# Kernel optimization log

Measured on AMD Instinct MI355X. Metric: run time of the kernel, lower is better.

## Reference

```python
import jax, jax.numpy as jnp
import numpy as np

N_USER = 100000
N_ITEM = 50000
N = N_USER + N_ITEM
E = 2400000
D = 64
L = 3
B = 4096
NEG_SLOPE = 0.01  # nn.LeakyReLU() default


def setup_inputs() -> dict:
    key = jax.random.key(0)
    ks = jax.random.split(key, 12)
    return {
        "features": jax.random.normal(ks[0], (N, D), dtype=jnp.float32),
        "rows": jax.random.randint(ks[1], (E,), 0, N),
        "cols": jax.random.randint(ks[2], (E,), 0, N),
        "vals": jax.random.uniform(ks[3], (E,), dtype=jnp.float32) * 0.02,
        "users": jax.random.randint(ks[4], (B,), 0, N_USER),
        "items": jax.random.randint(ks[5], (B,), 0, N_ITEM),
        "W1": jax.random.normal(ks[6], (L, D, D), dtype=jnp.float32) * 0.1,
        "b1": jax.random.normal(ks[7], (L, D), dtype=jnp.float32) * 0.01,
        "W2": jax.random.normal(ks[8], (L, D, D), dtype=jnp.float32) * 0.1,
        "b2": jax.random.normal(ks[9], (L, D), dtype=jnp.float32) * 0.01,
        "Wt": jax.random.normal(ks[10], (D, (L + 1) * D), dtype=jnp.float32) * 0.05,
        "bt": jax.random.normal(ks[11], (D,), dtype=jnp.float32) * 0.01,
    }


def _spmm(rows, cols, vals, x):
    # COO SpMM: out[r] += vals[e] * x[cols[e]]
    msgs = vals[:, None] * x[cols]  # [E, D] gather + scale
    return jax.ops.segment_sum(msgs, rows, num_segments=N)


def reference(features, rows, cols, vals, users, items, W1, b1, W2, b2, Wt, bt):
    feats = features
    embs = [feats]
    for l in range(L):
        agg = _spmm(rows, cols, vals, feats)          # sparse.mm(graph, features)
        part1 = (agg + feats) @ W1[l].T + b1[l]       # (graph+selfLoop) @ f -> Linear
        part2 = (agg * feats) @ W2[l].T + b2[l]       # elementwise mul -> Linear
        feats = jax.nn.leaky_relu(part1 + part2, negative_slope=NEG_SLOPE)
        embs.append(feats)
    final_emb = jnp.concatenate(embs, axis=1)         # [N, (L+1)*D]
    user_emb = final_emb[users] @ Wt.T + bt           # [B, D]
    item_emb = final_emb[N_USER + items] @ Wt.T + bt  # [B, D]
    return jnp.sum(user_emb * item_emb, axis=1)       # [B]
```

## Files before the change

### kernel.cpp

```cpp
#include <hip/hip_runtime.h>

#define N_USER 100000
#define N_NODE 150000
#define N_EDGE 2400000
#define DIM 64
#define BPAIR 4096
#define NEG_SLOPE 0.01f
#define RPG 4
#define NGROUP (N_NODE / RPG)
#define EPAD_CAP (N_EDGE + 8 * N_NODE)


__global__ void count_rank_kernel(const int* __restrict__ rows, int* __restrict__ cnt,
                                  int* __restrict__ rank) {
    int i = blockIdx.x * blockDim.x + threadIdx.x;
    if (i < N_EDGE) rank[i] = atomicAdd(&cnt[rows[i]], 1);
}

__global__ void scan1_kernel(const int* __restrict__ cnt, int* __restrict__ incl,
                             int* __restrict__ bsums) {
    __shared__ int s[256];
    int t = threadIdx.x;
    int i = blockIdx.x * 256 + t;
    s[t] = (i < N_NODE) ? ((cnt[i] + 7) & ~7) : 0;
    __syncthreads();
    for (int off = 1; off < 256; off <<= 1) {
        int add = (t >= off) ? s[t - off] : 0;
        __syncthreads();
        s[t] += add;
        __syncthreads();
    }
    if (i < N_NODE) incl[i] = s[t];
    if (t == 255) bsums[blockIdx.x] = s[255];
}

__global__ void scan2_kernel(int* __restrict__ bsums, int nblk) {
    __shared__ int s[1024];
    int t = threadIdx.x;
    s[t] = (t < nblk) ? bsums[t] : 0;
    __syncthreads();
    for (int off = 1; off < 1024; off <<= 1) {
        int add = (t >= off) ? s[t - off] : 0;
        __syncthreads();
        s[t] += add;
        __syncthreads();
    }
    if (t < nblk) bsums[t] = s[t];
}

__global__ void scan3_kernel(int* __restrict__ row_ptr, const int* __restrict__ bsums) {
    int i = blockIdx.x * 256 + threadIdx.x;
    if (i == 0) row_ptr[0] = 0;
    if (i < N_NODE && blockIdx.x > 0) row_ptr[1 + i] += bsums[blockIdx.x - 1];
}

__global__ void scatter_kernel(const int* __restrict__ rows, const int* __restrict__ cols,
                               const float* __restrict__ vals, const int* __restrict__ rank,
                               const int* __restrict__ row_ptr, int2* __restrict__ edges) {
    int i = blockIdx.x * blockDim.x + threadIdx.x;
    if (i < N_EDGE) {
        int p = row_ptr[rows[i]] + rank[i];
        edges[p] = make_int2(cols[i], __float_as_int(vals[i]));
    }
}

__global__ __launch_bounds__(256) void layer_kernel(
    const int* __restrict__ row_ptr, const int2* __restrict__ edges,
    const float* __restrict__ fin, float* __restrict__ fout,
    const float* __restrict__ W1l, const float* __restrict__ b1l,
    const float* __restrict__ W2l, const float* __restrict__ b2l) {
    __shared__ float h1s[4][RPG][64];
    __shared__ float h2s[4][RPG][64];
    int t = threadIdx.x;
    int wave = t >> 6, lane = t & 63;
    int gw = (blockIdx.x * 256 + t) >> 6;
    int nw = (gridDim.x * 256) >> 6;
    float bsum = b1l[lane] + b2l[lane];
    const float4* __restrict__ w1r = (const float4*)(W1l + (size_t)lane * 64);
    const float4* __restrict__ w2r = (const float4*)(W2l + (size_t)lane * 64);
    for (int g = gw; g < NGROUP; g += nw) {
        int r0 = g * RPG;
        int4 rp = *(const int4*)(row_ptr + r0);
        int rlast = row_ptr[r0 + 4];
        int eb[5] = {rp.x, rp.y, rp.z, rp.w, rlast};
#pragma unroll
        for (int m = 0; m < RPG; ++m) {
            int r = r0 + m;
            float f = fin[((size_t)r << 6) | lane];
            float a0 = 0.f, a1 = 0.f;
            for (int j = eb[m]; j < eb[m + 1]; j += 8) {
                int4 p0 = *(const int4*)(edges + j);
                int4 p1 = *(const int4*)(edges + j + 2);
                int4 p2 = *(const int4*)(edges + j + 4);
                int4 p3 = *(const int4*)(edges + j + 6);
                float g0 = fin[((size_t)p0.x << 6) | lane];
                float g1 = fin[((size_t)p0.z << 6) | lane];
                float g2 = fin[((size_t)p1.x << 6) | lane];
                float g3 = fin[((size_t)p1.z << 6) | lane];
                float g4 = fin[((size_t)p2.x << 6) | lane];
                float g5 = fin[((size_t)p2.z << 6) | lane];
                float g6 = fin[((size_t)p3.x << 6) | lane];
                float g7 = fin[((size_t)p3.z << 6) | lane];
                a0 += __int_as_float(p0.y) * g0;
                a1 += __int_as_float(p0.w) * g1;
                a0 += __int_as_float(p1.y) * g2;
                a1 += __int_as_float(p1.w) * g3;
                a0 += __int_as_float(p2.y) * g4;
                a1 += __int_as_float(p2.w) * g5;
                a0 += __int_as_float(p3.y) * g6;
                a1 += __int_as_float(p3.w) * g7;
            }
            float acc = a0 + a1;
            h1s[wave][m][lane] = acc + f;
            h2s[wave][m][lane] = acc * f;
        }
        float o0[RPG], o1[RPG];
#pragma unroll
        for (int m = 0; m < RPG; ++m) { o0[m] = bsum; o1[m] = 0.f; }
        const float4* h1r = (const float4*)&h1s[wave][0][0];
        const float4* h2r = (const float4*)&h2s[wave][0][0];
#pragma unroll 4
        for (int kk = 0; kk < 16; ++kk) {
            float4 w1v = w1r[kk];
            float4 w2v = w2r[kk];
#pragma unroll
            for (int m = 0; m < RPG; ++m) {
                float4 p = h1r[m * 16 + kk];
                float4 q = h2r[m * 16 + kk];
                o0[m] += w1v.x * p.x; o1[m] += w1v.y * p.y;
                o0[m] += w1v.z * p.z; o1[m] += w1v.w * p.w;
                o0[m] += w2v.x * q.x; o1[m] += w2v.y * q.y;
                o0[m] += w2v.z * q.z; o1[m] += w2v.w * q.w;
            }
        }
#pragma unroll
        for (int m = 0; m < RPG; ++m) {
            float o = o0[m] + o1[m];
            o = (o > 0.f) ? o : NEG_SLOPE * o;
            fout[((size_t)(r0 + m) << 6) | lane] = o;
        }
    }
}

__global__ void gather_kernel(float* __restrict__ dst, const float* __restrict__ src,
                              const int* __restrict__ users, const int* __restrict__ items) {
    int t = threadIdx.x;
    int p = blockIdx.x * 4 + (t >> 6);
    int lane = t & 63;
    if (p < 2 * BPAIR) {
        int node = (p < BPAIR) ? users[p] : (N_USER + items[p - BPAIR]);
        dst[((size_t)p << 6) | lane] = src[((size_t)node << 6) | lane];
    }
}

__global__ __launch_bounds__(256) void score_kernel(
    const float* __restrict__ features, const float* __restrict__ sel,
    const int* __restrict__ users, const int* __restrict__ items,
    const float* __restrict__ Wt, const float* __restrict__ bt,
    float* __restrict__ out) {
    __shared__ float hu[4][256];
    __shared__ float hv[4][256];
    int t = threadIdx.x;
    int wave = t >> 6, lane = t & 63;
    int gwave = (blockIdx.x * 256 + t) >> 6;
    int nwave = (gridDim.x * 256) >> 6;
    float btv = bt[lane];
    const float4* wrow = (const float4*)(Wt + (size_t)lane * 256);
    for (int p = gwave; p < BPAIR; p += nwave) {
        int u = users[p];
        int v = N_USER + items[p];
        hu[wave][lane] = features[((size_t)u << 6) | lane];
        hv[wave][lane] = features[((size_t)v << 6) | lane];
#pragma unroll
        for (int l = 0; l < 3; ++l) {
            hu[wave][64 + l * 64 + lane] = sel[(((size_t)l * 2 * BPAIR + p) << 6) | lane];
            hv[wave][64 + l * 64 + lane] = sel[(((size_t)l * 2 * BPAIR + BPAIR + p) << 6) | lane];
        }
        const float4* hu4 = (const float4*)&hu[wave][0];
        const float4* hv4 = (const float4*)&hv[wave][0];
        float pu0 = btv, pu1 = 0.f, pv0 = btv, pv1 = 0.f;
#pragma unroll 8
        for (int kk = 0; kk < 64; ++kk) {
            float4 w = wrow[kk];
            float4 a = hu4[kk];
            float4 b = hv4[kk];
            pu0 += w.x * a.x + w.z * a.z;
            pu1 += w.y * a.y + w.w * a.w;
            pv0 += w.x * b.x + w.z * b.z;
            pv1 += w.y * b.y + w.w * b.w;
        }
        float s = (pu0 + pu1) * (pv0 + pv1);
        for (int m = 32; m >= 1; m >>= 1) s += __shfl_xor(s, m, 64);
        if (lane == 0) out[p] = s;
    }
}

extern "C" void kernel_launch(void* const* d_in, const int* in_sizes, int n_in,
                              void* d_out, int out_size, void* d_ws, size_t ws_size,
                              hipStream_t stream) {
    const float* features = (const float*)d_in[0];
    const int*   rows     = (const int*)d_in[1];
    const int*   cols     = (const int*)d_in[2];
    const float* vals     = (const float*)d_in[3];
    const int*   users    = (const int*)d_in[4];
    const int*   items    = (const int*)d_in[5];
    const float* W1       = (const float*)d_in[6];
    const float* b1       = (const float*)d_in[7];
    const float* W2       = (const float*)d_in[8];
    const float* b2       = (const float*)d_in[9];
    const float* Wt       = (const float*)d_in[10];
    const float* bt       = (const float*)d_in[11];
    float* out = (float*)d_out;

    char* ws = (char*)d_ws;
    size_t off = 0;
    auto alloc = [&](size_t bytes) -> void* {
        void* p = ws + off;
        off += (bytes + 255) & ~(size_t)255;
        return p;
    };
    int*   row_ptr = (int*)alloc((N_NODE + 8) * sizeof(int));
    int*   cnt     = (int*)alloc(N_NODE * sizeof(int));
    int*   rank    = (int*)alloc((size_t)N_EDGE * sizeof(int));
    int*   bsums   = (int*)alloc(4096);
    int2*  edges   = (int2*)alloc((size_t)EPAD_CAP * sizeof(int2));
    float* f0      = (float*)alloc((size_t)N_NODE * DIM * sizeof(float));
    float* f1      = (float*)alloc((size_t)N_NODE * DIM * sizeof(float));
    float* sel     = (float*)alloc((size_t)3 * 2 * BPAIR * DIM * sizeof(float));

    hipMemsetAsync(cnt, 0, (size_t)N_NODE * sizeof(int), stream);
    hipMemsetAsync(edges, 0, (size_t)EPAD_CAP * sizeof(int2), stream);

    int eblocks = (N_EDGE + 255) / 256;
    int nblk = (N_NODE + 255) / 256;
    count_rank_kernel<<<eblocks, 256, 0, stream>>>(rows, cnt, rank);
    scan1_kernel<<<nblk, 256, 0, stream>>>(cnt, row_ptr + 1, bsums);
    scan2_kernel<<<1, 1024, 0, stream>>>(bsums, nblk);
    scan3_kernel<<<nblk, 256, 0, stream>>>(row_ptr, bsums);
    scatter_kernel<<<eblocks, 256, 0, stream>>>(rows, cols, vals, rank, row_ptr, edges);

    const float* fin = features;
    float* fbuf[2] = {f0, f1};
    for (int l = 0; l < 3; ++l) {
        float* fout = fbuf[l & 1];
        layer_kernel<<<2048, 256, 0, stream>>>(row_ptr, edges, fin, fout,
                                               W1 + (size_t)l * DIM * DIM, b1 + (size_t)l * DIM,
                                               W2 + (size_t)l * DIM * DIM, b2 + (size_t)l * DIM);
        gather_kernel<<<(2 * BPAIR) / 4, 256, 0, stream>>>(sel + (size_t)l * 2 * BPAIR * DIM,
                                                           fout, users, items);
        fin = fout;
    }
    score_kernel<<<256, 256, 0, stream>>>(features, sel, users, items, Wt, bt, out);
}
```

Before: 1.030 ms.

## Stage CSR edge chunks in LDS with register prefetch, 16 rows per wave

The layer kernel now gives each wave a contiguous block of 16 rows. It streams that block's padded edge list through LDS in 256-edge chunks, prefetching the next chunk into registers while the current one is processed, and crosses row boundaries without reloading. Dense transforms run in batches of 4 rows. This replaces per-row scalar int4 edge loads from global memory with coalesced chunk loads, and replaces the grid-stride persistent loop with one group per wave. The cost is more LDS per block and a boundary-check loop inside the edge loop, and a wave that draws a dense stretch of rows may lose load balance.

```diff
diff --git a/kernel.cpp b/kernel.cpp
--- a/kernel.cpp
+++ b/kernel.cpp
@@ -6,9 +6,10 @@
 #define DIM 64
 #define BPAIR 4096
 #define NEG_SLOPE 0.01f
-#define RPG 4
-#define NGROUP (N_NODE / RPG)
-#define EPAD_CAP (N_EDGE + 8 * N_NODE)
+#define RPW 16
+#define NG16 (N_NODE / RPW)
+#define CHUNK 256
+#define EPAD_CAP (N_EDGE + 8 * N_NODE + 2 * CHUNK)
 
 
 __global__ void count_rank_kernel(const int* __restrict__ rows, int* __restrict__ cnt,
@@ -69,54 +70,32 @@
     const float* __restrict__ fin, float* __restrict__ fout,
     const float* __restrict__ W1l, const float* __restrict__ b1l,
     const float* __restrict__ W2l, const float* __restrict__ b2l) {
-    __shared__ float h1s[4][RPG][64];
-    __shared__ float h2s[4][RPG][64];
-    int t = threadIdx.x;
-    int wave = t >> 6, lane = t & 63;
-    int gw = (blockIdx.x * 256 + t) >> 6;
-    int nw = (gridDim.x * 256) >> 6;
+    __shared__ int2  ebuf[4][CHUNK];
+    __shared__ float h1s[4][4][64];
+    __shared__ float h2s[4][4][64];
+    __shared__ int   rbnd[4][20];
+    int t = threadIdx.x, wave = t >> 6, lane = t & 63;
+    int g = blockIdx.x * 4 + wave;
+    if (g >= NG16) return;
+    int r0 = g * RPW;
     float bsum = b1l[lane] + b2l[lane];
     const float4* __restrict__ w1r = (const float4*)(W1l + (size_t)lane * 64);
     const float4* __restrict__ w2r = (const float4*)(W2l + (size_t)lane * 64);
-    for (int g = gw; g < NGROUP; g += nw) {
-        int r0 = g * RPG;
-        int4 rp = *(const int4*)(row_ptr + r0);
-        int rlast = row_ptr[r0 + 4];
-        int eb[5] = {rp.x, rp.y, rp.z, rp.w, rlast};
-#pragma unroll
-        for (int m = 0; m < RPG; ++m) {
-            int r = r0 + m;
-            float f = fin[((size_t)r << 6) | lane];
-            float a0 = 0.f, a1 = 0.f;
-            for (int j = eb[m]; j < eb[m + 1]; j += 8) {
-                int4 p0 = *(const int4*)(edges + j);
-                int4 p1 = *(const int4*)(edges + j + 2);
-                int4 p2 = *(const int4*)(edges + j + 4);
-                int4 p3 = *(const int4*)(edges + j + 6);
-                float g0 = fin[((size_t)p0.x << 6) | lane];
-                float g1 = fin[((size_t)p0.z << 6) | lane];
-                float g2 = fin[((size_t)p1.x << 6) | lane];
-                float g3 = fin[((size_t)p1.z << 6) | lane];
-                float g4 = fin[((size_t)p2.x << 6) | lane];
-                float g5 = fin[((size_t)p2.z << 6) | lane];
-                float g6 = fin[((size_t)p3.x << 6) | lane];
-                float g7 = fin[((size_t)p3.z << 6) | lane];
-                a0 += __int_as_float(p0.y) * g0;
-                a1 += __int_as_float(p0.w) * g1;
-                a0 += __int_as_float(p1.y) * g2;
-                a1 += __int_as_float(p1.w) * g3;
-                a0 += __int_as_float(p2.y) * g4;
-                a1 += __int_as_float(p2.w) * g5;
-                a0 += __int_as_float(p3.y) * g6;
-                a1 += __int_as_float(p3.w) * g7;
-            }
-            float acc = a0 + a1;
-            h1s[wave][m][lane] = acc + f;
-            h2s[wave][m][lane] = acc * f;
-        }
-        float o0[RPG], o1[RPG];
-#pragma unroll
-        for (int m = 0; m < RPG; ++m) { o0[m] = bsum; o1[m] = 0.f; }
+
+    if (lane < 17) rbnd[wave][lane] = row_ptr[r0 + lane];
+    int estart = rbnd[wave][0];
+    int eend   = rbnd[wave][16];
+    int nch = (eend - estart + CHUNK - 1) / CHUNK;
+
+    int m = 0;
+    int bnd = rbnd[wave][1];
+    float acc0 = 0.f, acc1 = 0.f;
+    float fcur = fin[((size_t)r0 << 6) | lane];
+
+    auto dense_batch = [&]() {
+        float o0[4], o1[4];
+#pragma unroll
+        for (int mm = 0; mm < 4; ++mm) { o0[mm] = bsum; o1[mm] = 0.f; }
         const float4* h1r = (const float4*)&h1s[wave][0][0];
         const float4* h2r = (const float4*)&h2s[wave][0][0];
 #pragma unroll 4
@@ -124,21 +103,78 @@
             float4 w1v = w1r[kk];
             float4 w2v = w2r[kk];
 #pragma unroll
-            for (int m = 0; m < RPG; ++m) {
-                float4 p = h1r[m * 16 + kk];
-                float4 q = h2r[m * 16 + kk];
-                o0[m] += w1v.x * p.x; o1[m] += w1v.y * p.y;
-                o0[m] += w1v.z * p.z; o1[m] += w1v.w * p.w;
-                o0[m] += w2v.x * q.x; o1[m] += w2v.y * q.y;
-                o0[m] += w2v.z * q.z; o1[m] += w2v.w * q.w;
+            for (int mm = 0; mm < 4; ++mm) {
+                float4 p = h1r[mm * 16 + kk];
+                float4 q = h2r[mm * 16 + kk];
+                o0[mm] += w1v.x * p.x; o1[mm] += w1v.y * p.y;
+                o0[mm] += w1v.z * p.z; o1[mm] += w1v.w * p.w;
+                o0[mm] += w2v.x * q.x; o1[mm] += w2v.y * q.y;
+                o0[mm] += w2v.z * q.z; o1[mm] += w2v.w * q.w;
             }
         }
-#pragma unroll
-        for (int m = 0; m < RPG; ++m) {
-            float o = o0[m] + o1[m];
+        int rb = r0 + m - 4;
+#pragma unroll
+        for (int mm = 0; mm < 4; ++mm) {
+            float o = o0[mm] + o1[mm];
             o = (o > 0.f) ? o : NEG_SLOPE * o;
-            fout[((size_t)(r0 + m) << 6) | lane] = o;
-        }
+            fout[((size_t)(rb + mm) << 6) | lane] = o;
+        }
+    };
+
+    const int2* ep = edges + estart;
+    int2 s0 = ep[lane], s1 = ep[lane + 64], s2 = ep[lane + 128], s3 = ep[lane + 192];
+
+    for (int c = 0; c < nch; ++c) {
+        int2* eb = &ebuf[wave][0];
+        eb[lane] = s0; eb[lane + 64] = s1; eb[lane + 128] = s2; eb[lane + 192] = s3;
+        if (c + 1 < nch) {
+            const int2* ep2 = edges + estart + (c + 1) * CHUNK;
+            s0 = ep2[lane]; s1 = ep2[lane + 64]; s2 = ep2[lane + 128]; s3 = ep2[lane + 192];
+        }
+        int cbase = estart + c * CHUNK;
+        int rem = eend - cbase;
+        int cnt = rem < CHUNK ? rem : CHUNK;
+        for (int k = 0; k < cnt; k += 8) {
+            while (cbase + k == bnd) {
+                float a = acc0 + acc1;
+                h1s[wave][m & 3][lane] = a + fcur;
+                h2s[wave][m & 3][lane] = a * fcur;
+                acc0 = 0.f; acc1 = 0.f;
+                ++m;
+                if ((m & 3) == 0) dense_batch();
+                fcur = fin[((size_t)(r0 + m) << 6) | lane];
+                bnd = rbnd[wave][m + 1];
+            }
+            int4 e01 = *(const int4*)(eb + k);
+            int4 e23 = *(const int4*)(eb + k + 2);
+            int4 e45 = *(const int4*)(eb + k + 4);
+            int4 e67 = *(const int4*)(eb + k + 6);
+            float g0 = fin[((size_t)e01.x << 6) | lane];
+            float g1 = fin[((size_t)e01.z << 6) | lane];
+            float g2 = fin[((size_t)e23.x << 6) | lane];
+            float g3 = fin[((size_t)e23.z << 6) | lane];
+            float g4 = fin[((size_t)e45.x << 6) | lane];
+            float g5 = fin[((size_t)e45.z << 6) | lane];
+            float g6 = fin[((size_t)e67.x << 6) | lane];
+            float g7 = fin[((size_t)e67.z << 6) | lane];
+            acc0 += __int_as_float(e01.y) * g0;
+            acc1 += __int_as_float(e01.w) * g1;
+            acc0 += __int_as_float(e23.y) * g2;
+            acc1 += __int_as_float(e23.w) * g3;
+            acc0 += __int_as_float(e45.y) * g4;
+            acc1 += __int_as_float(e45.w) * g5;
+            acc0 += __int_as_float(e67.y) * g6;
+            acc1 += __int_as_float(e67.w) * g7;
+        }
+    }
+    while (m < RPW) {
+        float a = acc0 + acc1;
+        h1s[wave][m & 3][lane] = a + fcur;
+        h2s[wave][m & 3][lane] = a * fcur;
+        acc0 = 0.f; acc1 = 0.f;
+        ++m;
+        if ((m & 3) == 0) dense_batch();
+        if (m < RPW) fcur = fin[((size_t)(r0 + m) << 6) | lane];
     }
 }
 
@@ -241,11 +277,12 @@
 
     const float* fin = features;
     float* fbuf[2] = {f0, f1};
+    int lblocks = (NG16 + 3) / 4;
     for (int l = 0; l < 3; ++l) {
         float* fout = fbuf[l & 1];
-        layer_kernel<<<2048, 256, 0, stream>>>(row_ptr, edges, fin, fout,
-                                               W1 + (size_t)l * DIM * DIM, b1 + (size_t)l * DIM,
-                                               W2 + (size_t)l * DIM * DIM, b2 + (size_t)l * DIM);
+        layer_kernel<<<lblocks, 256, 0, stream>>>(row_ptr, edges, fin, fout,
+                                                  W1 + (size_t)l * DIM * DIM, b1 + (size_t)l * DIM,
+                                                  W2 + (size_t)l * DIM * DIM, b2 + (size_t)l * DIM);
         gather_kernel<<<(2 * BPAIR) / 4, 256, 0, stream>>>(sel + (size_t)l * 2 * BPAIR * DIM,
                                                            fout, users, items);
         fin = fout;
```

Result: faster. 908.2 us (-11.8%).
